# Kernel tuning notes

Measured on AMD Instinct MI355X. Metric: run time of the kernel, lower is better.

## Reference

```python
import jax, jax.numpy as jnp
import numpy as np

ALPHA = 0.7
NUM_HEADS = 12
NUM_KV_HEADS = 6
HEAD_DIM = 64
ROPE_BASE = 10000.0


def ternary_quantize(w):
    thr = ALPHA * jnp.mean(jnp.abs(w))
    return jnp.sign(w) * (jnp.abs(w) >= thr).astype(w.dtype)


def bitlinear(x, w):
    # forward: F.linear(x, ternary(w)) * mean(|w|)
    scale = jnp.mean(jnp.abs(w))
    qw = ternary_quantize(w)
    return (x @ qw.T) * scale


def rope_tables(seq_len, dim, dtype):
    inv_freq = 1.0 / (ROPE_BASE ** (jnp.arange(0, dim, 2, dtype=jnp.float32) / dim))
    t = jnp.arange(seq_len, dtype=jnp.float32)
    freqs = jnp.outer(t, inv_freq)            # [S, dim/2]
    emb = jnp.concatenate([freqs, freqs], -1)  # [S, dim]
    return jnp.cos(emb).astype(dtype), jnp.sin(emb).astype(dtype)


def rotate_half(x):
    x1, x2 = jnp.split(x, 2, axis=-1)
    return jnp.concatenate([-x2, x1], axis=-1)


def setup_inputs() -> dict:
    key = jax.random.key(0)
    ks = jax.random.split(key, 5)
    B, S, H = 2, 2048, 768
    return {
        "hidden_states": jax.random.normal(ks[0], (B, S, H), jnp.float32),
        "Wq": jax.random.normal(ks[1], (768, 768), jnp.float32) * 0.02,
        "Wk": jax.random.normal(ks[2], (384, 768), jnp.float32) * 0.02,
        "Wv": jax.random.normal(ks[3], (384, 768), jnp.float32) * 0.02,
        "Wo": jax.random.normal(ks[4], (768, 768), jnp.float32) * 0.02,
    }


def reference(hidden_states, Wq, Wk, Wv, Wo):
    B, S, H = hidden_states.shape
    nh, nkv, hd = NUM_HEADS, NUM_KV_HEADS, HEAD_DIM
    groups = nh // nkv

    q = bitlinear(hidden_states, Wq).reshape(B, S, nh, hd).transpose(0, 2, 1, 3)
    k = bitlinear(hidden_states, Wk).reshape(B, S, nkv, hd).transpose(0, 2, 1, 3)
    v = bitlinear(hidden_states, Wv).reshape(B, S, nkv, hd).transpose(0, 2, 1, 3)

    cos, sin = rope_tables(S, hd, hidden_states.dtype)  # [S, hd]
    cos = cos[None, None]  # [1,1,S,hd]
    sin = sin[None, None]
    q = q * cos + rotate_half(q) * sin
    k = k * cos + rotate_half(k) * sin

    # GQA: expand kv heads to full head count
    k = jnp.repeat(k, groups, axis=1)  # [B, nh, S, hd]
    v = jnp.repeat(v, groups, axis=1)

    scale = 1.0 / jnp.sqrt(jnp.asarray(hd, hidden_states.dtype))
    scores = jnp.einsum("bhsd,bhtd->bhst", q, k) * scale
    attn = jax.nn.softmax(scores, axis=-1)
    out = jnp.einsum("bhst,bhtd->bhsd", attn, v)
    out = out.transpose(0, 2, 1, 3).reshape(B, S, H)
    return bitlinear(out, Wo)
```

## Files before the change

kernel.cpp:

```cpp
#include <hip/hip_runtime.h>
#include <cmath>

typedef unsigned short u16;
typedef unsigned int u32;
typedef __bf16 bf16x2 __attribute__((ext_vector_type(2)));
typedef __bf16 bf16x8 __attribute__((ext_vector_type(8)));
typedef float f32x2 __attribute__((ext_vector_type(2)));
typedef float f32x16 __attribute__((ext_vector_type(16)));

#define NQ (768*768)
#define NK (384*768)

__device__ __forceinline__ u16 f2bf(float f) {
  u32 u = __float_as_uint(f);
  u32 r = (u + 0x7FFFu + ((u >> 16) & 1u)) >> 16;
  return (u16)r;
}
__device__ __forceinline__ u32 packbf(float a, float b) {
#if __has_builtin(__builtin_amdgcn_cvt_pk_bf16_f32)
  bf16x2 v = __builtin_amdgcn_cvt_pk_bf16_f32(a, b);
  u32 r; __builtin_memcpy(&r, &v, 4); return r;
#else
  return (u32)f2bf(a) | ((u32)f2bf(b) << 16);
#endif
}
__device__ __forceinline__ float fexp2(float x) {
#if __has_builtin(__builtin_amdgcn_exp2f)
  return __builtin_amdgcn_exp2f(x);
#else
  return exp2f(x);
#endif
}
__device__ __forceinline__ bf16x8 ldfrag(const u16* p) { bf16x8 v; __builtin_memcpy(&v, p, 16); return v; }
__device__ __forceinline__ f32x16 mfma32_(bf16x8 a, bf16x8 b, f32x16 c) {
  return __builtin_amdgcn_mfma_f32_32x32x16_bf16(a, b, c, 0, 0, 0);
}
__device__ __forceinline__ void gload_lds16(const u16* g, u16* l) {
  __builtin_amdgcn_global_load_lds((const __attribute__((address_space(1))) void*)g,
                                   (__attribute__((address_space(3))) void*)l, 16, 0, 0);
}

__device__ __forceinline__ int fidx(int r, int k) {
  return (r >> 5) * 24576 + (k >> 4) * 512 + ((r & 31) + 32 * ((k >> 3) & 1)) * 8 + (k & 7);
}
__device__ __forceinline__ int kidx(int b6kvh, int s, int d) {
  return b6kvh * 131072 + (s >> 5) * 2048 + (d >> 4) * 512 +
         ((s & 31) + 32 * ((d >> 3) & 1)) * 8 + (d & 7);
}
__device__ __forceinline__ int qidx(int b, int s, int h, int d) {
  return ((b * 64 + (s >> 5)) * 12 + h) * 2048 + (d >> 4) * 512 +
         ((s & 31) + 32 * ((d >> 3) & 1)) * 8 + (d & 7);
}
__device__ __forceinline__ int vidx(int b6kvh, int d, int p) {
  return b6kvh * 131072 + (p >> 6) * 4096 + (d >> 5) * 2048 + ((p >> 4) & 3) * 512 +
         ((d & 31) + 32 * ((p >> 3) & 1)) * 8 + (p & 7);
}

__global__ __launch_bounds__(256) void abssum_kernel(const float* __restrict__ wq, const float* __restrict__ wk,
                                                     const float* __restrict__ wv, const float* __restrict__ wo,
                                                     float* __restrict__ sums) {
  int which = blockIdx.y;
  const float* w = (which == 0) ? wq : (which == 1) ? wk : (which == 2) ? wv : wo;
  int n4 = ((which == 0 || which == 3) ? NQ : NK) >> 2;
  const float4* w4 = (const float4*)w;
  float s = 0.f;
  for (int i = blockIdx.x * blockDim.x + threadIdx.x; i < n4; i += gridDim.x * blockDim.x) {
    float4 v = w4[i];
    s += fabsf(v.x) + fabsf(v.y) + fabsf(v.z) + fabsf(v.w);
  }
  for (int off = 32; off; off >>= 1) s += __shfl_down(s, off);
  __shared__ float ls[4];
  if ((threadIdx.x & 63) == 0) ls[threadIdx.x >> 6] = s;
  __syncthreads();
  if (threadIdx.x == 0) atomicAdd(&sums[which], ls[0] + ls[1] + ls[2] + ls[3]);
}

__global__ __launch_bounds__(256) void prep_kernel(const float* __restrict__ wq, const float* __restrict__ wk,
                                                   const float* __restrict__ wv, const float* __restrict__ wo,
                                                   const float* __restrict__ sums, const float* __restrict__ x,
                                                   u16* __restrict__ qw, u16* __restrict__ woq,
                                                   u16* __restrict__ xb, float2* __restrict__ rt) {
  int i = blockIdx.x * blockDim.x + threadIdx.x;
  if (i < 221184) {
    int n = i / 96, k8 = i - n * 96;
    const float* src; float th; u16* dst; int nd;
    if (n < 768)       { src = wq + n * 768;          th = 0.7f * sums[0] * (1.f / NQ); dst = qw;  nd = n; }
    else if (n < 1152) { src = wk + (n - 768) * 768;  th = 0.7f * sums[1] * (1.f / NK); dst = qw;  nd = n; }
    else if (n < 1536) { src = wv + (n - 1152) * 768; th = 0.7f * sums[2] * (1.f / NK); dst = qw;  nd = n; }
    else               { src = wo + (n - 1536) * 768; th = 0.7f * sums[3] * (1.f / NQ); dst = woq; nd = n - 1536; }
    const float4* sp = (const float4*)(src + k8 * 8);
    float4 v0 = sp[0], v1 = sp[1];
    float e[8] = {v0.x, v0.y, v0.z, v0.w, v1.x, v1.y, v1.z, v1.w};
    u16 o[8];
#pragma unroll
    for (int j = 0; j < 8; j++)
      o[j] = f2bf((fabsf(e[j]) >= th) ? ((e[j] > 0.f) ? 1.f : -1.f) : 0.f);
    __builtin_memcpy(dst + fidx(nd, k8 * 8), o, 16);
  } else if (i < 614400) {
    int j = i - 221184;
    int m = j / 96, k8 = j - m * 96;
    const float4* xp = (const float4*)(x + m * 768 + k8 * 8);
    float4 v0 = xp[0], v1 = xp[1];
    u16 o[8] = { f2bf(v0.x), f2bf(v0.y), f2bf(v0.z), f2bf(v0.w),
                 f2bf(v1.x), f2bf(v1.y), f2bf(v1.z), f2bf(v1.w) };
    __builtin_memcpy(xb + fidx(m, k8 * 8), o, 16);
  } else {
    int j = i - 614400;
    int s = j >> 5, c = j & 31;
    float f = exp2f((float)c * -0.41524101186092029f);
    float sn, cs; sincosf((float)s * f, &sn, &cs);
    rt[j] = make_float2(cs, sn);
  }
}

__global__ __launch_bounds__(256, 2) void gemm_qkv_kernel(const u16* __restrict__ xb, const u16* __restrict__ qw,
                                                          const float* __restrict__ sums,
                                                          const float2* __restrict__ rt,
                                                          u16* __restrict__ qb, u16* __restrict__ kb,
                                                          u16* __restrict__ vT) {
  __shared__ u16 sA[2][4][4][512];
  __shared__ u16 sB[2][4][4][512];
  int tn = blockIdx.x, tm = blockIdx.y;
  int t = threadIdx.x, lane = t & 63, w = t >> 6, c = lane & 31, g2 = lane >> 5;
  int wm = w & 1, wn = w >> 1;

  const u16* asrc = xb + (tm * 4 + w) * 24576 + lane * 8;
  const u16* bsrc = qw + (tn * 4 + w) * 24576 + lane * 8;

  auto stage = [&](int s, int bufi) {
    u16* adst = &sA[bufi][w][0][0];
    u16* bdst = &sB[bufi][w][0][0];
    const u16* ap = asrc + s * 2048;
    const u16* bp = bsrc + s * 2048;
#pragma unroll
    for (int kc = 0; kc < 4; kc++) {
      gload_lds16(ap + kc * 512, adst + kc * 512);
      gload_lds16(bp + kc * 512, bdst + kc * 512);
    }
  };

  f32x16 acc[2][2];
  acc[0][0] = (f32x16)0.f; acc[0][1] = (f32x16)0.f;
  acc[1][0] = (f32x16)0.f; acc[1][1] = (f32x16)0.f;

  stage(0, 0);
  __syncthreads();
  for (int s = 0; s < 12; ++s) {
    int b = s & 1;
    if (s < 11) stage(s + 1, b ^ 1);
#pragma unroll
    for (int kc = 0; kc < 4; kc++) {
      bf16x8 a0 = ldfrag(&sA[b][2 * wm][kc][lane * 8]);
      bf16x8 a1 = ldfrag(&sA[b][2 * wm + 1][kc][lane * 8]);
      bf16x8 b0 = ldfrag(&sB[b][2 * wn][kc][lane * 8]);
      bf16x8 b1 = ldfrag(&sB[b][2 * wn + 1][kc][lane * 8]);
      acc[0][0] = mfma32_(a0, b0, acc[0][0]);
      acc[0][1] = mfma32_(a0, b1, acc[0][1]);
      acc[1][0] = mfma32_(a1, b0, acc[1][0]);
      acc[1][1] = mfma32_(a1, b1, acc[1][1]);
    }
    __syncthreads();
  }

  float sq = sums[0] * (1.f / NQ) * 0.180336880111120f;
  float sk = sums[1] * (1.f / NK);
  float sv = sums[2] * (1.f / NK);
  if (tn < 9) {
    float sc = (tn < 6) ? sq : sk;
    int head = (tn < 6) ? (tn * 2 + wn) : ((tn - 6) * 2 + wn);
    const float2* rp = rt + c;
#pragma unroll
    for (int mi = 0; mi < 2; mi++) {
      int mb = tm * 128 + wm * 64 + mi * 32 + 4 * g2;
#pragma unroll
      for (int r = 0; r < 16; r++) {
        int m = mb + (r & 3) + 8 * (r >> 2);
        int bb = m >> 11, s = m & 2047;
        float2 cs2 = rp[s << 5];
        float x1 = acc[mi][0][r] * sc, x2 = acc[mi][1][r] * sc;
        u16 y1 = f2bf(x1 * cs2.x - x2 * cs2.y);
        u16 y2 = f2bf(x2 * cs2.x + x1 * cs2.y);
        if (tn < 6) {
          qb[qidx(bb, s, head, c)]      = y1;
          qb[qidx(bb, s, head, c + 32)] = y2;
        } else {
          kb[kidx(bb * 6 + head, s, c)]      = y1;
          kb[kidx(bb * 6 + head, s, c + 32)] = y2;
        }
      }
    }
  } else {
    int kvh = (tn - 9) * 2 + wn;
#pragma unroll
    for (int mi = 0; mi < 2; mi++) {
      int mb = tm * 128 + wm * 64 + mi * 32 + 4 * g2;
#pragma unroll
      for (int nb = 0; nb < 2; nb++)
#pragma unroll
        for (int r = 0; r < 16; r++) {
          int m = mb + (r & 3) + 8 * (r >> 2);
          int bb = m >> 11, s = m & 2047;
          int sp = (s & ~12) | ((s & 4) << 1) | ((s & 8) >> 1);
          vT[vidx(bb * 6 + kvh, nb * 32 + c, sp)] = f2bf(acc[mi][nb][r] * sv);
        }
    }
  }
}

__device__ __forceinline__ void attn_step(const bf16x8 (&kf)[4], const bf16x8 (&vf)[2][2],
                                          const bf16x8 (&qf)[4], f32x16 (&O)[2], float& lsum) {
  f32x16 S = (f32x16)0.f;
  __builtin_amdgcn_s_setprio(1);
#pragma unroll
  for (int ks = 0; ks < 4; ks++) S = mfma32_(kf[ks], qf[ks], S);
  __builtin_amdgcn_s_setprio(0);
#pragma unroll
  for (int r = 0; r < 16; r++) S[r] = fexp2(S[r]);
  f32x2 a0 = {S[0], S[1]},  a1 = {S[2], S[3]},  a2 = {S[4], S[5]},  a3 = {S[6], S[7]};
  f32x2 a4 = {S[8], S[9]},  a5 = {S[10], S[11]}, a6 = {S[12], S[13]}, a7 = {S[14], S[15]};
  f32x2 b0 = a0 + a1, b1 = a2 + a3, b2 = a4 + a5, b3 = a6 + a7;
  f32x2 c0 = b0 + b1, c1 = b2 + b3;
  f32x2 d = c0 + c1;
  lsum += d.x + d.y;
  u32 P[8];
#pragma unroll
  for (int j = 0; j < 8; j++) P[j] = packbf(S[2 * j], S[2 * j + 1]);
  bf16x8 PA0, PA1;
  __builtin_memcpy(&PA0, &P[0], 16);
  __builtin_memcpy(&PA1, &P[4], 16);
  __builtin_amdgcn_s_setprio(1);
  O[0] = mfma32_(PA0, vf[0][0], O[0]);
  O[1] = mfma32_(PA0, vf[1][0], O[1]);
  O[0] = mfma32_(PA1, vf[0][1], O[0]);
  O[1] = mfma32_(PA1, vf[1][1], O[1]);
  __builtin_amdgcn_s_setprio(0);
}

__global__ __launch_bounds__(256, 3) void attn_kernel(const u16* __restrict__ qb, const u16* __restrict__ kb,
                                                      const u16* __restrict__ vT, u16* __restrict__ ab) {
  __shared__ float Obuf[4][32][66];
  __shared__ float Lbuf[4][32];
  int bk = blockIdx.x;
  int b = bk / 6, kvh = bk % 6;
  int qp = blockIdx.y & 31, h2 = blockIdx.y >> 5;
  int h = kvh * 2 + h2;
  int t = threadIdx.x, lane = t & 63, w = t >> 6, c = lane & 31, g2 = lane >> 5;

  const u16* q0 = qb + ((b * 64 + qp * 2) * 12 + h) * 2048 + lane * 8;
  const u16* q1 = q0 + 12 * 2048;
  bf16x8 qf0[4], qf1[4];
#pragma unroll
  for (int ks = 0; ks < 4; ks++) { qf0[ks] = ldfrag(q0 + ks * 512); qf1[ks] = ldfrag(q1 + ks * 512); }

  f32x16 fz = (f32x16)0.f;
  f32x16 O0[2] = {fz, fz}, O1[2] = {fz, fz};
  float lsum0 = 0.f, lsum1 = 0.f;

  const u16* Kb = kb + bk * 131072;
  const u16* Vb = vT + bk * 131072;

  for (int it = 0; it < 16; ++it) {
    int g = w * 16 + it;
    const u16* kt = Kb + g * 2048 + lane * 8;
    const u16* vt = Vb + (g >> 1) * 4096 + (g & 1) * 1024 + lane * 8;
    bf16x8 kf[4], vf[2][2];
#pragma unroll
    for (int ks = 0; ks < 4; ks++) kf[ks] = ldfrag(kt + ks * 512);
#pragma unroll
    for (int dn = 0; dn < 2; dn++)
#pragma unroll
      for (int ksv = 0; ksv < 2; ksv++)
        vf[dn][ksv] = ldfrag(vt + dn * 2048 + ksv * 512);
    attn_step(kf, vf, qf0, O0, lsum0);
    attn_step(kf, vf, qf1, O1, lsum1);
  }

  float lt0 = lsum0 + __shfl_xor(lsum0, 32);
  float lt1 = lsum1 + __shfl_xor(lsum1, 32);

#pragma unroll
  for (int qi = 0; qi < 2; qi++) {
    if (qi) __syncthreads();
    if (g2 == 0) Lbuf[w][c] = qi ? lt1 : lt0;
    const f32x16* Ow = qi ? O1 : O0;
#pragma unroll
    for (int dn = 0; dn < 2; dn++)
#pragma unroll
      for (int r = 0; r < 16; r++)
        Obuf[w][(r & 3) + 8 * (r >> 2) + 4 * g2][dn * 32 + c] = Ow[dn][r];
    __syncthreads();
    int qq = t >> 3, col8 = (t & 7) * 8;
    float l = Lbuf[0][qq] + Lbuf[1][qq] + Lbuf[2][qq] + Lbuf[3][qq];
    float inv = 1.f / l;
    u16 o[8];
#pragma unroll
    for (int j = 0; j < 8; j++)
      o[j] = f2bf((Obuf[0][qq][col8 + j] + Obuf[1][qq][col8 + j] +
                   Obuf[2][qq][col8 + j] + Obuf[3][qq][col8 + j]) * inv);
    int mg = b * 64 + qp * 2 + qi;
    u16* dst = ab + mg * 24576 + ((h * 64 + col8) >> 4) * 512 + ((col8 >> 3) & 1) * 256 + qq * 8;
    __builtin_memcpy(dst, o, 16);
  }
}

__global__ __launch_bounds__(256, 3) void gemm_out_kernel(const u16* __restrict__ ab, const u16* __restrict__ woq,
                                                          const float* __restrict__ sums, float* __restrict__ out) {
  int tn = blockIdx.x, tm = blockIdx.y;
  int t = threadIdx.x, lane = t & 63, w = t >> 6, c = lane & 31, g2 = lane >> 5;
  int wm = w & 1, wn = w >> 1;
  const u16* abase = ab + (tm * 2 + wm) * 24576 + lane * 8;
  const u16* bbase = woq + (tn * 2 + wn) * 24576 + lane * 8;
  f32x16 acc = (f32x16)0.f;
  bf16x8 aA[4], bA[4], aB[4], bB[4];
#pragma unroll
  for (int ks = 0; ks < 4; ks++) {
    aA[ks] = ldfrag(abase + ks * 512);
    bA[ks] = ldfrag(bbase + ks * 512);
  }
#pragma unroll
  for (int kk = 0; kk < 48; kk += 8) {
#pragma unroll
    for (int ks = 0; ks < 4; ks++) {
      aB[ks] = ldfrag(abase + (kk + 4 + ks) * 512);
      bB[ks] = ldfrag(bbase + (kk + 4 + ks) * 512);
    }
#pragma unroll
    for (int ks = 0; ks < 4; ks++) acc = mfma32_(aA[ks], bA[ks], acc);
    if (kk + 8 < 48) {
#pragma unroll
      for (int ks = 0; ks < 4; ks++) {
        aA[ks] = ldfrag(abase + (kk + 8 + ks) * 512);
        bA[ks] = ldfrag(bbase + (kk + 8 + ks) * 512);
      }
    }
#pragma unroll
    for (int ks = 0; ks < 4; ks++) acc = mfma32_(aB[ks], bB[ks], acc);
  }
  float so = sums[3] * (1.f / NQ);
  int mb = tm * 64 + wm * 32 + 4 * g2;
#pragma unroll
  for (int r = 0; r < 16; r++) {
    int m = mb + (r & 3) + 8 * (r >> 2);
    out[m * 768 + tn * 64 + wn * 32 + c] = acc[r] * so;
  }
}

extern "C" void kernel_launch(void* const* d_in, const int* in_sizes, int n_in,
                              void* d_out, int out_size, void* d_ws, size_t ws_size,
                              hipStream_t stream) {
  const float* x  = (const float*)d_in[0];
  const float* wq = (const float*)d_in[1];
  const float* wk = (const float*)d_in[2];
  const float* wv = (const float*)d_in[3];
  const float* wo = (const float*)d_in[4];
  float* out = (float*)d_out;
  char* ws = (char*)d_ws;

  float* sums = (float*)ws;
  u16* qw  = (u16*)(ws + 256);
  u16* woq = (u16*)(ws + 2359552);
  u16* xb  = (u16*)(ws + 3539200);
  u16* qb  = (u16*)(ws + 9830656);
  u16* kb  = (u16*)(ws + 16122112);
  u16* vT  = (u16*)(ws + 19267840);
  u16* ab  = (u16*)(ws + 22413568);
  float2* rt = (float2*)(ws + 28705024);

  hipMemsetAsync(sums, 0, 16, stream);
  dim3 blk(256);
  abssum_kernel<<<dim3(64, 4), blk, 0, stream>>>(wq, wk, wv, wo, sums);
  prep_kernel<<<dim3(2656), blk, 0, stream>>>(wq, wk, wv, wo, sums, x, qw, woq, xb, rt);
  gemm_qkv_kernel<<<dim3(12, 32), blk, 0, stream>>>(xb, qw, sums, rt, qb, kb, vT);
  attn_kernel<<<dim3(12, 64), blk, 0, stream>>>(qb, kb, vT, ab);
  gemm_out_kernel<<<dim3(12, 64), blk, 0, stream>>>(ab, woq, sums, out);
}
```

Baseline: 153.4 us.

## Split attention waves by query tile and stage output GEMM through LDS

The attention kernel now gives each wave a single query tile and half the key range, instead of two query tiles over a quarter of the keys. This halves the register accumulators and raises launch bounds to allow more resident blocks, at the cost of each wave loading more K/V fragments. The output projection GEMM now uses 128-row tiles with double-buffered global-to-LDS loads, so B fragments are shared across waves and the grid is halved. That adds barriers and LDS traffic.

```diff
diff --git a/kernel.cpp b/kernel.cpp
--- a/kernel.cpp
+++ b/kernel.cpp
@@ -236,7 +236,7 @@
   __builtin_amdgcn_s_setprio(0);
 }
 
-__global__ __launch_bounds__(256, 3) void attn_kernel(const u16* __restrict__ qb, const u16* __restrict__ kb,
+__global__ __launch_bounds__(256, 4) void attn_kernel(const u16* __restrict__ qb, const u16* __restrict__ kb,
                                                       const u16* __restrict__ vT, u16* __restrict__ ab) {
   __shared__ float Obuf[4][32][66];
   __shared__ float Lbuf[4][32];
@@ -245,22 +245,23 @@
   int qp = blockIdx.y & 31, h2 = blockIdx.y >> 5;
   int h = kvh * 2 + h2;
   int t = threadIdx.x, lane = t & 63, w = t >> 6, c = lane & 31, g2 = lane >> 5;
-
-  const u16* q0 = qb + ((b * 64 + qp * 2) * 12 + h) * 2048 + lane * 8;
-  const u16* q1 = q0 + 12 * 2048;
-  bf16x8 qf0[4], qf1[4];
-#pragma unroll
-  for (int ks = 0; ks < 4; ks++) { qf0[ks] = ldfrag(q0 + ks * 512); qf1[ks] = ldfrag(q1 + ks * 512); }
+  int qi = w & 1, kh = w >> 1;
+  int qt = qp * 2 + qi;
+
+  const u16* qbase = qb + ((b * 64 + qt) * 12 + h) * 2048 + lane * 8;
+  bf16x8 qf[4];
+#pragma unroll
+  for (int ks = 0; ks < 4; ks++) qf[ks] = ldfrag(qbase + ks * 512);
 
   f32x16 fz = (f32x16)0.f;
-  f32x16 O0[2] = {fz, fz}, O1[2] = {fz, fz};
-  float lsum0 = 0.f, lsum1 = 0.f;
+  f32x16 O[2] = {fz, fz};
+  float lsum = 0.f;
 
   const u16* Kb = kb + bk * 131072;
   const u16* Vb = vT + bk * 131072;
 
-  for (int it = 0; it < 16; ++it) {
-    int g = w * 16 + it;
+  for (int it = 0; it < 32; ++it) {
+    int g = kh * 32 + it;
     const u16* kt = Kb + g * 2048 + lane * 8;
     const u16* vt = Vb + (g >> 1) * 4096 + (g & 1) * 1024 + lane * 8;
     bf16x8 kf[4], vf[2][2];
@@ -271,77 +272,82 @@
 #pragma unroll
       for (int ksv = 0; ksv < 2; ksv++)
         vf[dn][ksv] = ldfrag(vt + dn * 2048 + ksv * 512);
-    attn_step(kf, vf, qf0, O0, lsum0);
-    attn_step(kf, vf, qf1, O1, lsum1);
-  }
-
-  float lt0 = lsum0 + __shfl_xor(lsum0, 32);
-  float lt1 = lsum1 + __shfl_xor(lsum1, 32);
-
-#pragma unroll
-  for (int qi = 0; qi < 2; qi++) {
-    if (qi) __syncthreads();
-    if (g2 == 0) Lbuf[w][c] = qi ? lt1 : lt0;
-    const f32x16* Ow = qi ? O1 : O0;
-#pragma unroll
-    for (int dn = 0; dn < 2; dn++)
-#pragma unroll
-      for (int r = 0; r < 16; r++)
-        Obuf[w][(r & 3) + 8 * (r >> 2) + 4 * g2][dn * 32 + c] = Ow[dn][r];
-    __syncthreads();
-    int qq = t >> 3, col8 = (t & 7) * 8;
-    float l = Lbuf[0][qq] + Lbuf[1][qq] + Lbuf[2][qq] + Lbuf[3][qq];
+    attn_step(kf, vf, qf, O, lsum);
+  }
+
+  float ltot = lsum + __shfl_xor(lsum, 32);
+  if (g2 == 0) Lbuf[w][c] = ltot;
+#pragma unroll
+  for (int dn = 0; dn < 2; dn++)
+#pragma unroll
+    for (int r = 0; r < 16; r++)
+      Obuf[w][(r & 3) + 8 * (r >> 2) + 4 * g2][dn * 32 + c] = O[dn][r];
+  __syncthreads();
+  {
+    int hn = t >> 7, qq = (t >> 2) & 31, dc = (t & 3) * 16;
+    float l = Lbuf[hn][qq] + Lbuf[hn + 2][qq];
     float inv = 1.f / l;
-    u16 o[8];
-#pragma unroll
-    for (int j = 0; j < 8; j++)
-      o[j] = f2bf((Obuf[0][qq][col8 + j] + Obuf[1][qq][col8 + j] +
-                   Obuf[2][qq][col8 + j] + Obuf[3][qq][col8 + j]) * inv);
-    int mg = b * 64 + qp * 2 + qi;
-    u16* dst = ab + mg * 24576 + ((h * 64 + col8) >> 4) * 512 + ((col8 >> 3) & 1) * 256 + qq * 8;
+    u16 o[16];
+#pragma unroll
+    for (int j = 0; j < 16; j++)
+      o[j] = f2bf((Obuf[hn][qq][dc + j] + Obuf[hn + 2][qq][dc + j]) * inv);
+    int mg = b * 64 + qp * 2 + hn;
+    u16* dst = ab + mg * 24576 + ((h * 64 + dc) >> 4) * 512 + qq * 8;
     __builtin_memcpy(dst, o, 16);
+    __builtin_memcpy(dst + 256, o + 8, 16);
   }
 }
 
 __global__ __launch_bounds__(256, 3) void gemm_out_kernel(const u16* __restrict__ ab, const u16* __restrict__ woq,
                                                           const float* __restrict__ sums, float* __restrict__ out) {
+  __shared__ u16 sA[2][4][4][512];
+  __shared__ u16 sB[2][2][4][512];
   int tn = blockIdx.x, tm = blockIdx.y;
   int t = threadIdx.x, lane = t & 63, w = t >> 6, c = lane & 31, g2 = lane >> 5;
   int wm = w & 1, wn = w >> 1;
-  const u16* abase = ab + (tm * 2 + wm) * 24576 + lane * 8;
-  const u16* bbase = woq + (tn * 2 + wn) * 24576 + lane * 8;
-  f32x16 acc = (f32x16)0.f;
-  bf16x8 aA[4], bA[4], aB[4], bB[4];
-#pragma unroll
-  for (int ks = 0; ks < 4; ks++) {
-    aA[ks] = ldfrag(abase + ks * 512);
-    bA[ks] = ldfrag(bbase + ks * 512);
-  }
-#pragma unroll
-  for (int kk = 0; kk < 48; kk += 8) {
-#pragma unroll
-    for (int ks = 0; ks < 4; ks++) {
-      aB[ks] = ldfrag(abase + (kk + 4 + ks) * 512);
-      bB[ks] = ldfrag(bbase + (kk + 4 + ks) * 512);
-    }
-#pragma unroll
-    for (int ks = 0; ks < 4; ks++) acc = mfma32_(aA[ks], bA[ks], acc);
-    if (kk + 8 < 48) {
-#pragma unroll
-      for (int ks = 0; ks < 4; ks++) {
-        aA[ks] = ldfrag(abase + (kk + 8 + ks) * 512);
-        bA[ks] = ldfrag(bbase + (kk + 8 + ks) * 512);
-      }
-    }
-#pragma unroll
-    for (int ks = 0; ks < 4; ks++) acc = mfma32_(aB[ks], bB[ks], acc);
-  }
+
+  const u16* asrc = ab + (tm * 4 + w) * 24576 + lane * 8;
+  const u16* bsrc = woq + (tn * 2 + (w >> 1)) * 24576 + lane * 8;
+  int kc0 = (w & 1) * 2;
+
+  auto stage = [&](int s, int bufi) {
+    const u16* ap = asrc + s * 2048;
+    u16* adst = &sA[bufi][w][0][0];
+#pragma unroll
+    for (int kc = 0; kc < 4; kc++) gload_lds16(ap + kc * 512, adst + kc * 512);
+    const u16* bp = bsrc + s * 2048;
+    u16* bdst = &sB[bufi][w >> 1][0][0];
+#pragma unroll
+    for (int j = 0; j < 2; j++) gload_lds16(bp + (kc0 + j) * 512, bdst + (kc0 + j) * 512);
+  };
+
+  f32x16 acc[2]; acc[0] = (f32x16)0.f; acc[1] = (f32x16)0.f;
+
+  stage(0, 0);
+  __syncthreads();
+  for (int s = 0; s < 12; ++s) {
+    int b = s & 1;
+    if (s < 11) stage(s + 1, b ^ 1);
+#pragma unroll
+    for (int kc = 0; kc < 4; kc++) {
+      bf16x8 a0 = ldfrag(&sA[b][2 * wm][kc][lane * 8]);
+      bf16x8 a1 = ldfrag(&sA[b][2 * wm + 1][kc][lane * 8]);
+      bf16x8 bf = ldfrag(&sB[b][wn][kc][lane * 8]);
+      acc[0] = mfma32_(a0, bf, acc[0]);
+      acc[1] = mfma32_(a1, bf, acc[1]);
+    }
+    __syncthreads();
+  }
+
   float so = sums[3] * (1.f / NQ);
-  int mb = tm * 64 + wm * 32 + 4 * g2;
-#pragma unroll
-  for (int r = 0; r < 16; r++) {
-    int m = mb + (r & 3) + 8 * (r >> 2);
-    out[m * 768 + tn * 64 + wn * 32 + c] = acc[r] * so;
+#pragma unroll
+  for (int mi = 0; mi < 2; mi++) {
+    int mb = tm * 128 + wm * 64 + mi * 32 + 4 * g2;
+#pragma unroll
+    for (int r = 0; r < 16; r++) {
+      int m = mb + (r & 3) + 8 * (r >> 2);
+      out[m * 768 + tn * 64 + wn * 32 + c] = acc[mi][r] * so;
+    }
   }
 }
 
@@ -372,5 +378,5 @@
   prep_kernel<<<dim3(2656), blk, 0, stream>>>(wq, wk, wv, wo, sums, x, qw, woq, xb, rt);
   gemm_qkv_kernel<<<dim3(12, 32), blk, 0, stream>>>(xb, qw, sums, rt, qb, kb, vT);
   attn_kernel<<<dim3(12, 64), blk, 0, stream>>>(qb, kb, vT, ab);
-  gemm_out_kernel<<<dim3(12, 64), blk, 0, stream>>>(ab, woq, sums, out);
-}
+  gemm_out_kernel<<<dim3(12, 32), blk, 0, stream>>>(ab, woq, sums, out);
+}
```

Result: slower. 157.9 us (+3.0%).

## Shrink QKV GEMM tile, drop double buffering, and add XCD-aware block swizzle

Applied to the files above, without the earlier changes.

The QKV GEMM moves from a 128x128 tile with double-buffered LDS to a 64x128 tile with a single LDS buffer. This doubles the grid to 768 blocks and raises the occupancy hint to 3, trading less intra-block overlap and less reuse for more parallelism. All three main kernels now launch a 1D grid of 768 blocks, remapped so consecutive tiles land on the same XCD to improve L2 locality. Without the prefetch stage, each k-step waits on its own loads, so global-load latency is exposed more.

```diff
diff --git a/kernel.cpp b/kernel.cpp
--- a/kernel.cpp
+++ b/kernel.cpp
@@ -39,6 +39,7 @@
   __builtin_amdgcn_global_load_lds((const __attribute__((address_space(1))) void*)g,
                                    (__attribute__((address_space(3))) void*)l, 16, 0, 0);
 }
+__device__ __forceinline__ int xcd_swz768(int lin) { return (lin & 7) * 96 + (lin >> 3); }
 
 __device__ __forceinline__ int fidx(int r, int k) {
   return (r >> 5) * 24576 + (k >> 4) * 512 + ((r & 31) + 32 * ((k >> 3) & 1)) * 8 + (k & 7);
@@ -113,51 +114,37 @@
   }
 }
 
-__global__ __launch_bounds__(256, 2) void gemm_qkv_kernel(const u16* __restrict__ xb, const u16* __restrict__ qw,
+__global__ __launch_bounds__(256, 3) void gemm_qkv_kernel(const u16* __restrict__ xb, const u16* __restrict__ qw,
                                                           const float* __restrict__ sums,
                                                           const float2* __restrict__ rt,
                                                           u16* __restrict__ qb, u16* __restrict__ kb,
                                                           u16* __restrict__ vT) {
-  __shared__ u16 sA[2][4][4][512];
-  __shared__ u16 sB[2][4][4][512];
-  int tn = blockIdx.x, tm = blockIdx.y;
+  __shared__ u16 sm[24 * 512];
+  int v = xcd_swz768(blockIdx.x);
+  int tm = v / 12, tn = v - tm * 12;
   int t = threadIdx.x, lane = t & 63, w = t >> 6, c = lane & 31, g2 = lane >> 5;
   int wm = w & 1, wn = w >> 1;
-
-  const u16* asrc = xb + (tm * 4 + w) * 24576 + lane * 8;
-  const u16* bsrc = qw + (tn * 4 + w) * 24576 + lane * 8;
-
-  auto stage = [&](int s, int bufi) {
-    u16* adst = &sA[bufi][w][0][0];
-    u16* bdst = &sB[bufi][w][0][0];
-    const u16* ap = asrc + s * 2048;
-    const u16* bp = bsrc + s * 2048;
+  int wn8 = wn * 8;
+
+  f32x16 acc[2]; acc[0] = (f32x16)0.f; acc[1] = (f32x16)0.f;
+
+  for (int s = 0; s < 12; ++s) {
+#pragma unroll
+    for (int i = 0; i < 6; i++) {
+      int ch = w * 6 + i;
+      const u16* src = (ch < 8)
+        ? xb + (tm * 2 + (ch >> 2)) * 24576 + (s * 4 + (ch & 3)) * 512 + lane * 8
+        : qw + (tn * 4 + (ch >> 2) - 2) * 24576 + (s * 4 + (ch & 3)) * 512 + lane * 8;
+      gload_lds16(src, sm + ch * 512);
+    }
+    __syncthreads();
 #pragma unroll
     for (int kc = 0; kc < 4; kc++) {
-      gload_lds16(ap + kc * 512, adst + kc * 512);
-      gload_lds16(bp + kc * 512, bdst + kc * 512);
-    }
-  };
-
-  f32x16 acc[2][2];
-  acc[0][0] = (f32x16)0.f; acc[0][1] = (f32x16)0.f;
-  acc[1][0] = (f32x16)0.f; acc[1][1] = (f32x16)0.f;
-
-  stage(0, 0);
-  __syncthreads();
-  for (int s = 0; s < 12; ++s) {
-    int b = s & 1;
-    if (s < 11) stage(s + 1, b ^ 1);
-#pragma unroll
-    for (int kc = 0; kc < 4; kc++) {
-      bf16x8 a0 = ldfrag(&sA[b][2 * wm][kc][lane * 8]);
-      bf16x8 a1 = ldfrag(&sA[b][2 * wm + 1][kc][lane * 8]);
-      bf16x8 b0 = ldfrag(&sB[b][2 * wn][kc][lane * 8]);
-      bf16x8 b1 = ldfrag(&sB[b][2 * wn + 1][kc][lane * 8]);
-      acc[0][0] = mfma32_(a0, b0, acc[0][0]);
-      acc[0][1] = mfma32_(a0, b1, acc[0][1]);
-      acc[1][0] = mfma32_(a1, b0, acc[1][0]);
-      acc[1][1] = mfma32_(a1, b1, acc[1][1]);
+      bf16x8 a  = ldfrag(sm + (wm * 4 + kc) * 512 + lane * 8);
+      bf16x8 b0 = ldfrag(sm + (8 + wn8 + kc) * 512 + lane * 8);
+      bf16x8 b1 = ldfrag(sm + (12 + wn8 + kc) * 512 + lane * 8);
+      acc[0] = mfma32_(a, b0, acc[0]);
+      acc[1] = mfma32_(a, b1, acc[1]);
     }
     __syncthreads();
   }
@@ -165,45 +152,38 @@
   float sq = sums[0] * (1.f / NQ) * 0.180336880111120f;
   float sk = sums[1] * (1.f / NK);
   float sv = sums[2] * (1.f / NK);
+  int mb = tm * 64 + wm * 32 + 4 * g2;
   if (tn < 9) {
     float sc = (tn < 6) ? sq : sk;
     int head = (tn < 6) ? (tn * 2 + wn) : ((tn - 6) * 2 + wn);
     const float2* rp = rt + c;
 #pragma unroll
-    for (int mi = 0; mi < 2; mi++) {
-      int mb = tm * 128 + wm * 64 + mi * 32 + 4 * g2;
+    for (int r = 0; r < 16; r++) {
+      int m = mb + (r & 3) + 8 * (r >> 2);
+      int bb = m >> 11, s = m & 2047;
+      float2 cs2 = rp[s << 5];
+      float x1 = acc[0][r] * sc, x2 = acc[1][r] * sc;
+      u16 y1 = f2bf(x1 * cs2.x - x2 * cs2.y);
+      u16 y2 = f2bf(x2 * cs2.x + x1 * cs2.y);
+      if (tn < 6) {
+        qb[qidx(bb, s, head, c)]      = y1;
+        qb[qidx(bb, s, head, c + 32)] = y2;
+      } else {
+        kb[kidx(bb * 6 + head, s, c)]      = y1;
+        kb[kidx(bb * 6 + head, s, c + 32)] = y2;
+      }
+    }
+  } else {
+    int kvh = (tn - 9) * 2 + wn;
+#pragma unroll
+    for (int nb = 0; nb < 2; nb++)
 #pragma unroll
       for (int r = 0; r < 16; r++) {
         int m = mb + (r & 3) + 8 * (r >> 2);
         int bb = m >> 11, s = m & 2047;
-        float2 cs2 = rp[s << 5];
-        float x1 = acc[mi][0][r] * sc, x2 = acc[mi][1][r] * sc;
-        u16 y1 = f2bf(x1 * cs2.x - x2 * cs2.y);
-        u16 y2 = f2bf(x2 * cs2.x + x1 * cs2.y);
-        if (tn < 6) {
-          qb[qidx(bb, s, head, c)]      = y1;
-          qb[qidx(bb, s, head, c + 32)] = y2;
-        } else {
-          kb[kidx(bb * 6 + head, s, c)]      = y1;
-          kb[kidx(bb * 6 + head, s, c + 32)] = y2;
-        }
+        int sp = (s & ~12) | ((s & 4) << 1) | ((s & 8) >> 1);
+        vT[vidx(bb * 6 + kvh, nb * 32 + c, sp)] = f2bf(acc[nb][r] * sv);
       }
-    }
-  } else {
-    int kvh = (tn - 9) * 2 + wn;
-#pragma unroll
-    for (int mi = 0; mi < 2; mi++) {
-      int mb = tm * 128 + wm * 64 + mi * 32 + 4 * g2;
-#pragma unroll
-      for (int nb = 0; nb < 2; nb++)
-#pragma unroll
-        for (int r = 0; r < 16; r++) {
-          int m = mb + (r & 3) + 8 * (r >> 2);
-          int bb = m >> 11, s = m & 2047;
-          int sp = (s & ~12) | ((s & 4) << 1) | ((s & 8) >> 1);
-          vT[vidx(bb * 6 + kvh, nb * 32 + c, sp)] = f2bf(acc[mi][nb][r] * sv);
-        }
-    }
   }
 }
 
@@ -240,9 +220,10 @@
                                                       const u16* __restrict__ vT, u16* __restrict__ ab) {
   __shared__ float Obuf[4][32][66];
   __shared__ float Lbuf[4][32];
-  int bk = blockIdx.x;
+  int v = xcd_swz768(blockIdx.x);
+  int bk = v >> 6, y = v & 63;
   int b = bk / 6, kvh = bk % 6;
-  int qp = blockIdx.y & 31, h2 = blockIdx.y >> 5;
+  int qp = y & 31, h2 = y >> 5;
   int h = kvh * 2 + h2;
   int t = threadIdx.x, lane = t & 63, w = t >> 6, c = lane & 31, g2 = lane >> 5;
 
@@ -305,7 +286,8 @@
 
 __global__ __launch_bounds__(256, 3) void gemm_out_kernel(const u16* __restrict__ ab, const u16* __restrict__ woq,
                                                           const float* __restrict__ sums, float* __restrict__ out) {
-  int tn = blockIdx.x, tm = blockIdx.y;
+  int v = xcd_swz768(blockIdx.x);
+  int tm = v / 12, tn = v - tm * 12;
   int t = threadIdx.x, lane = t & 63, w = t >> 6, c = lane & 31, g2 = lane >> 5;
   int wm = w & 1, wn = w >> 1;
   const u16* abase = ab + (tm * 2 + wm) * 24576 + lane * 8;
@@ -370,7 +352,7 @@
   dim3 blk(256);
   abssum_kernel<<<dim3(64, 4), blk, 0, stream>>>(wq, wk, wv, wo, sums);
   prep_kernel<<<dim3(2656), blk, 0, stream>>>(wq, wk, wv, wo, sums, x, qw, woq, xb, rt);
-  gemm_qkv_kernel<<<dim3(12, 32), blk, 0, stream>>>(xb, qw, sums, rt, qb, kb, vT);
-  attn_kernel<<<dim3(12, 64), blk, 0, stream>>>(qb, kb, vT, ab);
-  gemm_out_kernel<<<dim3(12, 64), blk, 0, stream>>>(ab, woq, sums, out);
-}
+  gemm_qkv_kernel<<<dim3(768), blk, 0, stream>>>(xb, qw, sums, rt, qb, kb, vT);
+  attn_kernel<<<dim3(768), blk, 0, stream>>>(qb, kb, vT, ab);
+  gemm_out_kernel<<<dim3(768), blk, 0, stream>>>(ab, woq, sums, out);
+}
```

Result: faster. 149.6 us (-2.5%).
